# Kernel optimization log

Measured on AMD Instinct MI355X. Metric: run time of the kernel, lower is better.

## Reference

```python
import jax, jax.numpy as jnp
import numpy as np

IN, H, L, T = 44, 128, 4, 50  # input_size, hidden_size, num_layers, target_len
B, S = 2048, 200


def _lstm_cell(xt, h, c, Wih, Whh, b):
    # xt [B,in], h/c [B,H]; Wih [4H,in], Whh [4H,H], b [4H] (b_ih+b_hh fused)
    gates = xt @ Wih.T + h @ Whh.T + b
    i, f, g, o = jnp.split(gates, 4, axis=-1)
    c_new = jax.nn.sigmoid(f) * c + jax.nn.sigmoid(i) * jnp.tanh(g)
    h_new = jax.nn.sigmoid(o) * jnp.tanh(c_new)
    return h_new, c_new


def _run_layer(xs, Wih, Whh, b):
    # xs [S,B,in] -> ys [S,B,H], final (h,c)
    Bn = xs.shape[1]
    h0 = jnp.zeros((Bn, H), xs.dtype)
    c0 = jnp.zeros((Bn, H), xs.dtype)

    def step(carry, xt):
        h, c = carry
        h, c = _lstm_cell(xt, h, c, Wih, Whh, b)
        return (h, c), h

    (hT, cT), ys = jax.lax.scan(step, (h0, c0), xs)
    return ys, hT, cT


def setup_inputs() -> dict:
    key = jax.random.key(0)
    ks = jax.random.split(key, 16)
    s = 1.0 / np.sqrt(H)
    u = lambda k, shape: jax.random.uniform(k, shape, jnp.float32, -s, s)
    return {
        "x": jax.random.normal(ks[0], (B, S, IN), jnp.float32),
        "target": jax.random.normal(ks[1], (B, T, IN), jnp.float32),
        "enc_Wih0": u(ks[2], (4 * H, IN)),
        "enc_WihR": u(ks[3], (L - 1, 4 * H, H)),
        "enc_Whh": u(ks[4], (L, 4 * H, H)),
        "enc_b": u(ks[5], (L, 4 * H)),
        "dec_Wih0": u(ks[6], (4 * H, IN)),
        "dec_WihR": u(ks[7], (L - 1, 4 * H, H)),
        "dec_Whh": u(ks[8], (L, 4 * H, H)),
        "dec_b": u(ks[9], (L, 4 * H)),
        "fc_W": u(ks[10], (IN, H)),
        "fc_b": u(ks[11], (IN,)),
    }


def reference(x, target, enc_Wih0, enc_WihR, enc_Whh, enc_b,
              dec_Wih0, dec_WihR, dec_Whh, dec_b, fc_W, fc_b):
    # ---- encoder: 4-layer LSTM over the source sequence ----
    xs = jnp.transpose(x, (1, 0, 2))  # [S,B,IN]
    ys, h, c = _run_layer(xs, enc_Wih0, enc_Whh[0], enc_b[0])
    hs, cs = [h], [c]
    for l in range(1, L):
        ys, h, c = _run_layer(ys, enc_WihR[l - 1], enc_Whh[l], enc_b[l])
        hs.append(h)
        cs.append(c)
    hs = jnp.stack(hs)  # [L,B,H]
    cs = jnp.stack(cs)

    # ---- decoder: recursive decode for T steps (seq_len=1 per step) ----
    dec_in0 = x[:, -1, :]  # [B,IN]

    def dec_step(carry, _):
        dec_in, hsc, csc = carry
        new_h, new_c = [], []
        inp = dec_in
        for l in range(L):
            Wih = dec_Wih0 if l == 0 else dec_WihR[l - 1]
            hl, cl = _lstm_cell(inp, hsc[l], csc[l], Wih, dec_Whh[l], dec_b[l])
            new_h.append(hl)
            new_c.append(cl)
            inp = hl
        out = inp @ fc_W.T + fc_b  # [B,IN]
        return (out, jnp.stack(new_h), jnp.stack(new_c)), out

    _, outs = jax.lax.scan(dec_step, (dec_in0, hs, cs), None, length=T)
    return jnp.transpose(outs, (1, 0, 2))  # [B,T,IN]
```

## Files before the change

### kernel.cpp

```cpp
#include <hip/hip_runtime.h>
#include <hip/hip_bf16.h>
#include <cstdint>
#include <cstddef>

typedef _Float16 half8  __attribute__((ext_vector_type(8)));
typedef float    floatx4 __attribute__((ext_vector_type(4)));
typedef int      int4v   __attribute__((ext_vector_type(4)));

#define S_LEN 200
#define BATCH 2048
#define HID   128
#define T_LEN 50
#define IN_D  44

#define SENT32 0x7E007E00

#define OFF_ENCW   0ull
#define OFF_DECW   983040ull
#define OFF_RING_E 1978368ull
#define OFF_RING_D 14561280ull
#define OFF_ORING  20852736ull
#define OFF_HENC   21901312ull
#define OFF_CENC   23998464ull
#define OFF_FLAGS  28192768ull

#define SCOPE_AGENT __HIP_MEMORY_SCOPE_AGENT

#define LOG2E  1.44269504f
#define LOG2E2 2.88539008f
__device__ __forceinline__ float sigf(float x){
  float e = __builtin_amdgcn_exp2f(-LOG2E * x);
  return __builtin_amdgcn_rcpf(1.f + e);
}
__device__ __forceinline__ float tanhf_fast(float x){
  float e = __builtin_amdgcn_exp2f(LOG2E2 * x);
  return 1.f - 2.f * __builtin_amdgcn_rcpf(e + 1.f);
}

__device__ __forceinline__ int  ldc(const int* p){ return __hip_atomic_load(p, __ATOMIC_RELAXED, SCOPE_AGENT); }
__device__ __forceinline__ void stc(int* p, int v){ __hip_atomic_store(p, v, __ATOMIC_RELAXED, SCOPE_AGENT); }
__device__ __forceinline__ void drain_vm(){ asm volatile("s_waitcnt vmcnt(0)" ::: "memory"); }
__device__ __forceinline__ int* flagp(int* flags, int idx){ return flags + idx*32; }

__device__ __forceinline__ int4v ld_ring_x4(const int* p){
  int4v r;
  asm volatile("global_load_dwordx4 %0, %1, off sc0 sc1\n\t"
               "s_waitcnt vmcnt(0)"
               : "=v"(r) : "v"(p) : "memory");
  return r;
}
__device__ __forceinline__ void st_ring_x4(int* p, int4v v){
  asm volatile("global_store_dwordx4 %0, %1, off sc0 sc1"
               :: "v"(p), "v"(v) : "memory");
}
__device__ __forceinline__ bool any_sent(int4v v){
  return (v.x==SENT32)||(v.y==SENT32)||(v.z==SENT32)||(v.w==SENT32);
}

#define PIN(v) asm volatile("" : "+v"(v))

__global__ void prep_weights(const float* __restrict__ eW0, const float* __restrict__ eWR,
                             const float* __restrict__ eWH, const float* __restrict__ dW0,
                             const float* __restrict__ dWR, const float* __restrict__ dWH,
                             const float* __restrict__ fcW,
                             _Float16* __restrict__ encw, _Float16* __restrict__ decw,
                             int* __restrict__ rings, int* __restrict__ flags)
{
  int i = blockIdx.x*256 + threadIdx.x;
  if (i < 491520) {
    _Float16 v;
    if (i < 32768)      { int j=i>>6, k=i&63; v = (k<IN_D)? (_Float16)eW0[j*IN_D+k] : (_Float16)0.f; }
    else if (i < 229376){ v = (_Float16)eWR[i-32768]; }
    else                { v = (_Float16)eWH[i-229376]; }
    encw[i] = v;
  }
  if (i < 497664) {
    _Float16 v;
    if (i < 32768)      { int j=i>>6, k=i&63; v = (k<IN_D)? (_Float16)dW0[j*IN_D+k] : (_Float16)0.f; }
    else if (i < 229376){ v = (_Float16)dWR[i-32768]; }
    else if (i < 491520){ v = (_Float16)dWH[i-229376]; }
    else { int r=i-491520; int j=r>>7, k=r&127; v = (j<IN_D)? (_Float16)fcW[j*HID+k] : (_Float16)0.f; }
    decw[i] = v;
  }
  for (int j = i; j < 4980736; j += 4096*256) rings[j] = SENT32;
  if (i < 32768) flags[i] = 0;
}


__global__ __launch_bounds__(512, 2)
void enc_pipe(const float* __restrict__ x, const _Float16* __restrict__ encw,
              const float* __restrict__ enc_b, _Float16* __restrict__ ring,
              _Float16* __restrict__ h_enc, float* __restrict__ c_enc,
              int* __restrict__ flags)
{
  const int tid = threadIdx.x;
  const int w = tid >> 6, lane = tid & 63, quad = lane >> 4, n16 = lane & 15;
  const int l = blockIdx.x >> 6, s = blockIdx.x & 63, r0 = s * 32;
  const int u = w*16 + n16;
  const int KSI = (l == 0) ? 2 : 4;

  __shared__ _Float16 xbuf[32][136];
  __shared__ _Float16 hb[2][32][136];

  for (int i = tid; i < 32*136; i += 512){
    ((_Float16*)xbuf)[i] = (_Float16)0.f;
    ((_Float16*)hb[0])[i] = (_Float16)0.f;
  }

  const _Float16* Wi = (l==0) ? encw : encw + 32768 + (size_t)(l-1)*65536;
  const _Float16* Wh = encw + 229376 + (size_t)l*65536;
  const int KI = KSI * 32;
  floatx4 wfi[4][4], wfh[4][4];
  #pragma unroll
  for (int nt = 0; nt < 4; ++nt){
    const int grow = nt*128 + u;
    #pragma unroll
    for (int ks = 0; ks < 4; ++ks){
      if (ks < KSI){ wfi[nt][ks] = *(const floatx4*)(Wi + (size_t)grow*KI + ks*32 + quad*8); PIN(wfi[nt][ks]); }
      wfh[nt][ks] = *(const floatx4*)(Wh + (size_t)grow*HID + ks*32 + quad*8); PIN(wfh[nt][ks]);
    }
  }
  float breg[4];
  #pragma unroll
  for (int g = 0; g < 4; ++g) breg[g] = enc_b[l*512 + g*128 + u];
  float creg[2][4] = {{0.f,0.f,0.f,0.f},{0.f,0.f,0.f,0.f}};

  int xr_r[3], xr_k[3]; bool xr_v[3]; float xr[3];
  if (l == 0){
    #pragma unroll
    for (int j = 0; j < 3; ++j){
      int idx = tid + j*512; xr_v[j] = idx < 32*IN_D;
      xr_r[j] = xr_v[j] ? idx / IN_D : 0; xr_k[j] = xr_v[j] ? idx % IN_D : 0;
      xr[j] = xr_v[j] ? x[((size_t)(r0+xr_r[j])*S_LEN + 0)*IN_D + xr_k[j]] : 0.f;
    }
  }

  int* cflag_self = flagp(flags, l*64 + s);
  int* cflag_next = flagp(flags, (l+1)*64 + s);
  int seen_cons = 0;

  __syncthreads();

  _Float16 (*hcur)[136] = hb[0];
  _Float16 (*hnxt)[136] = hb[1];

  const int d0 = tid, d1 = tid+512, d2 = tid+1024, d3 = tid+1536;

  for (int t = 0; t < S_LEN; ++t){
    if (l == 0){
      #pragma unroll
      for (int j = 0; j < 3; ++j)
        if (xr_v[j]) xbuf[xr_r[j]][xr_k[j]] = (_Float16)xr[j];
    } else {
      int* srcd = (int*)(ring + (((size_t)(l-1)*8 + (t&7))*BATCH + r0)*HID);
      int v0 = ldc(srcd+d0), v1 = ldc(srcd+d1), v2 = ldc(srcd+d2), v3 = ldc(srcd+d3);
      while (v0==SENT32 || v1==SENT32 || v2==SENT32 || v3==SENT32){
        if (v0==SENT32) v0 = ldc(srcd+d0);
        if (v1==SENT32) v1 = ldc(srcd+d1);
        if (v2==SENT32) v2 = ldc(srcd+d2);
        if (v3==SENT32) v3 = ldc(srcd+d3);
      }
      *(int*)&xbuf[d0>>6][(d0&63)*2] = v0;
      *(int*)&xbuf[d1>>6][(d1&63)*2] = v1;
      *(int*)&xbuf[d2>>6][(d2&63)*2] = v2;
      *(int*)&xbuf[d3>>6][(d3&63)*2] = v3;
      stc(srcd+d0, SENT32); stc(srcd+d1, SENT32);
      stc(srcd+d2, SENT32); stc(srcd+d3, SENT32);
    }
    if (tid == 0 && l < 3 && t >= 8){
      while (seen_cons < t-7){
        seen_cons = ldc(cflag_next);
        if (seen_cons < t-7) __builtin_amdgcn_s_sleep(1);
      }
    }
    __syncthreads();

    if (l == 0 && t < S_LEN-1){
      #pragma unroll
      for (int j = 0; j < 3; ++j)
        if (xr_v[j]) xr[j] = x[((size_t)(r0+xr_r[j])*S_LEN + (t+1))*IN_D + xr_k[j]];
    }

    #pragma unroll
    for (int m = 0; m < 2; ++m){
      half8 ai[4], ah[4];
      #pragma unroll
      for (int ks = 0; ks < 4; ++ks){
        if (ks < KSI) ai[ks] = *(const half8*)&xbuf[m*16+n16][ks*32 + quad*8];
        ah[ks] = *(const half8*)&hcur[m*16+n16][ks*32 + quad*8];
      }
      floatx4 acc[4];
      #pragma unroll
      for (int nt = 0; nt < 4; ++nt){
        acc[nt] = (floatx4){0.f,0.f,0.f,0.f};
        #pragma unroll
        for (int ks = 0; ks < 4; ++ks){
          if (ks < KSI) acc[nt] = __builtin_amdgcn_mfma_f32_16x16x32_f16(ai[ks], __builtin_bit_cast(half8, wfi[nt][ks]), acc[nt], 0,0,0);
          acc[nt] = __builtin_amdgcn_mfma_f32_16x16x32_f16(ah[ks], __builtin_bit_cast(half8, wfh[nt][ks]), acc[nt], 0,0,0);
        }
      }
      #pragma unroll
      for (int rr = 0; rr < 4; ++rr){
        float ip = acc[0][rr] + breg[0];
        float fp = acc[1][rr] + breg[1];
        float gp = acc[2][rr] + breg[2];
        float op = acc[3][rr] + breg[3];
        float cc = sigf(fp)*creg[m][rr] + sigf(ip)*tanhf_fast(gp);
        float hh = sigf(op)*tanhf_fast(cc);
        creg[m][rr] = cc;
        const int row = m*16 + quad*4 + rr;
        hnxt[row][u] = (_Float16)hh;
        if (t == S_LEN-1){
          h_enc[((size_t)l*BATCH + r0 + row)*HID + u] = (_Float16)hh;
          c_enc[((size_t)l*BATCH + r0 + row)*HID + u] = cc;
        }
      }
    }
    __syncthreads();

    if (l > 0){
      drain_vm();
      if (tid == 0) stc(cflag_self, t+1);
    }
    if (l < 3){
      int* dst = (int*)(ring + (((size_t)l*8 + (t&7))*BATCH + r0)*HID);
      stc(dst+d0, *(const int*)&hnxt[d0>>6][(d0&63)*2]);
      stc(dst+d1, *(const int*)&hnxt[d1>>6][(d1&63)*2]);
      stc(dst+d2, *(const int*)&hnxt[d2>>6][(d2&63)*2]);
      stc(dst+d3, *(const int*)&hnxt[d3>>6][(d3&63)*2]);
    }
    _Float16 (*tmp)[136] = hcur; hcur = hnxt; hnxt = tmp;
  }
}


__global__ __launch_bounds__(512, 2)
void dec_pipe(const float* __restrict__ x, const _Float16* __restrict__ decw,
              const float* __restrict__ dec_b, const float* __restrict__ fc_b,
              _Float16* __restrict__ ring, _Float16* __restrict__ oring,
              const _Float16* __restrict__ h_enc, const float* __restrict__ c_enc,
              int* __restrict__ flags, float* __restrict__ out)
{
  const int tid = threadIdx.x;
  const int w = tid >> 6, lane = tid & 63, quad = lane >> 4, n16 = lane & 15;
  const int l = blockIdx.x >> 6, s = blockIdx.x & 63, r0 = s * 32;
  const int u = w*16 + n16;
  const int KSI = (l == 0) ? 2 : 4;
  const int my4 = tid*4;

  __shared__ _Float16 xbuf[32][136];
  __shared__ _Float16 hb[2][32][136];
  __shared__ _Float16 fcout[32][64];

  for (int i = tid; i < 32*136; i += 512) ((_Float16*)xbuf)[i] = (_Float16)0.f;
  for (int i = tid; i < 32*64; i += 512) ((_Float16*)fcout)[i] = (_Float16)0.f;

  const _Float16* Wi = (l==0) ? decw : decw + 32768 + (size_t)(l-1)*65536;
  const _Float16* Wh = decw + 229376 + (size_t)l*65536;
  const _Float16* FCW = decw + 491520;
  const int KI = KSI * 32;
  floatx4 wfi[4][4], wfh[4][4];
  #pragma unroll
  for (int nt = 0; nt < 4; ++nt){
    const int grow = nt*128 + u;
    #pragma unroll
    for (int ks = 0; ks < 4; ++ks){
      if (ks < KSI){ wfi[nt][ks] = *(const floatx4*)(Wi + (size_t)grow*KI + ks*32 + quad*8); PIN(wfi[nt][ks]); }
      wfh[nt][ks] = *(const floatx4*)(Wh + (size_t)grow*HID + ks*32 + quad*8); PIN(wfh[nt][ks]);
    }
  }
  float breg[4];
  #pragma unroll
  for (int g = 0; g < 4; ++g) breg[g] = dec_b[l*512 + g*128 + u];

  {
    int idx = tid*8, rr_ = idx >> 7, kk = idx & 127;
    *(half8*)&hb[0][rr_][kk] = *(const half8*)(h_enc + ((size_t)l*BATCH + r0)*HID + rr_*HID + kk);
  }
  float creg[2][4];
  #pragma unroll
  for (int m = 0; m < 2; ++m)
    #pragma unroll
    for (int rr = 0; rr < 4; ++rr)
      creg[m][rr] = c_enc[((size_t)l*BATCH + r0 + m*16 + quad*4 + rr)*HID + u];

  floatx4 wfc[4]; float fcb_j = 0.f;
  const int j = w*16 + n16;
  if (w < 3){
    #pragma unroll
    for (int ks = 0; ks < 4; ++ks){
      wfc[ks] = *(const floatx4*)(FCW + (size_t)j*HID + ks*32 + quad*8); PIN(wfc[ks]);
    }
    if (j < IN_D) fcb_j = fc_b[j];
  }

  int* cflag_self = flagp(flags, 256 + l*64 + s);
  int* cflag_next = flagp(flags, 256 + (l+1)*64 + s);
  int* cflag_o    = flagp(flags, 512 + s);
  int seen = 0;

  __syncthreads();

  _Float16 (*hcur)[136] = hb[0];
  _Float16 (*hnxt)[136] = hb[1];

  const int4v sv = {SENT32, SENT32, SENT32, SENT32};

  for (int t = 0; t < T_LEN; ++t){
    if (l == 0){
      if (t == 0){
        for (int idx = tid; idx < 32*IN_D; idx += 512){
          int r = idx / IN_D, k = idx % IN_D;
          xbuf[r][k] = (_Float16)x[((size_t)(r0+r)*S_LEN + (S_LEN-1))*IN_D + k];
        }
      } else if (tid < 256){
        int* srcd = (int*)(oring + (((size_t)((t-1)&3))*BATCH + r0)*64);
        int4v v = ld_ring_x4(srcd + my4);
        while (any_sent(v)){
          __builtin_amdgcn_s_sleep(1);
          v = ld_ring_x4(srcd + my4);
        }
        *(int4v*)&xbuf[my4>>5][(my4&31)*2] = v;
        st_ring_x4(srcd + my4, sv);
      }
    } else {
      int* srcd = (int*)(ring + (((size_t)(l-1)*4 + (t&3))*BATCH + r0)*HID);
      int4v v = ld_ring_x4(srcd + my4);
      while (any_sent(v)){
        __builtin_amdgcn_s_sleep(1);
        v = ld_ring_x4(srcd + my4);
      }
      *(int4v*)&xbuf[my4>>6][(my4&63)*2] = v;
      st_ring_x4(srcd + my4, sv);
    }
    if (tid == 0 && t >= 4){
      if (l < 3){
        while (seen < t-3){ seen = ldc(cflag_next); if (seen < t-3) __builtin_amdgcn_s_sleep(1); }
      } else {
        while (seen < t-2){ seen = ldc(cflag_o); if (seen < t-2) __builtin_amdgcn_s_sleep(1); }
      }
    }
    __syncthreads();

    #pragma unroll
    for (int m = 0; m < 2; ++m){
      half8 ai[4], ah[4];
      #pragma unroll
      for (int ks = 0; ks < 4; ++ks){
        if (ks < KSI) ai[ks] = *(const half8*)&xbuf[m*16+n16][ks*32 + quad*8];
        ah[ks] = *(const half8*)&hcur[m*16+n16][ks*32 + quad*8];
      }
      floatx4 acc[4];
      #pragma unroll
      for (int nt = 0; nt < 4; ++nt){
        acc[nt] = (floatx4){0.f,0.f,0.f,0.f};
        #pragma unroll
        for (int ks = 0; ks < 4; ++ks){
          if (ks < KSI) acc[nt] = __builtin_amdgcn_mfma_f32_16x16x32_f16(ai[ks], __builtin_bit_cast(half8, wfi[nt][ks]), acc[nt], 0,0,0);
          acc[nt] = __builtin_amdgcn_mfma_f32_16x16x32_f16(ah[ks], __builtin_bit_cast(half8, wfh[nt][ks]), acc[nt], 0,0,0);
        }
      }
      #pragma unroll
      for (int rr = 0; rr < 4; ++rr){
        float ip = acc[0][rr] + breg[0];
        float fp = acc[1][rr] + breg[1];
        float gp = acc[2][rr] + breg[2];
        float op = acc[3][rr] + breg[3];
        float cc = sigf(fp)*creg[m][rr] + sigf(ip)*tanhf_fast(gp);
        float hh = sigf(op)*tanhf_fast(cc);
        creg[m][rr] = cc;
        hnxt[m*16 + quad*4 + rr][u] = (_Float16)hh;
      }
    }
    __syncthreads();

    drain_vm();
    if (tid == 0){
      if (l > 0) stc(cflag_self, t+1);
      else if (t > 0) stc(cflag_o, t+1);
    }

    if (l < 3){
      int* dst = (int*)(ring + (((size_t)l*4 + (t&3))*BATCH + r0)*HID);
      st_ring_x4(dst + my4, *(const int4v*)&hnxt[my4>>6][(my4&63)*2]);
    } else {
      if (w < 3){
        #pragma unroll
        for (int m = 0; m < 2; ++m){
          half8 a3[4];
          #pragma unroll
          for (int ks = 0; ks < 4; ++ks) a3[ks] = *(const half8*)&hnxt[m*16+n16][ks*32 + quad*8];
          floatx4 facc = (floatx4){0.f,0.f,0.f,0.f};
          #pragma unroll
          for (int ks = 0; ks < 4; ++ks) facc = __builtin_amdgcn_mfma_f32_16x16x32_f16(a3[ks], __builtin_bit_cast(half8, wfc[ks]), facc, 0,0,0);
          #pragma unroll
          for (int rr = 0; rr < 4; ++rr){
            const int row = m*16 + quad*4 + rr;
            float v = facc[rr] + fcb_j;
            fcout[row][j] = (_Float16)v;
            if (j < IN_D)
              out[((size_t)(r0 + row)*T_LEN + t)*IN_D + j] = v;
          }
        }
      }
      __syncthreads();
      if (tid < 256){
        int* odst = (int*)(oring + (((size_t)(t&3))*BATCH + r0)*64);
        st_ring_x4(odst + my4, *(const int4v*)&fcout[my4>>5][(my4&31)*2]);
      }
    }
    _Float16 (*tmp)[136] = hcur; hcur = hnxt; hnxt = tmp;
  }
  drain_vm();
}

extern "C" void kernel_launch(void* const* d_in, const int* in_sizes, int n_in,
                              void* d_out, int out_size, void* d_ws, size_t ws_size,
                              hipStream_t stream)
{
  const float* x        = (const float*)d_in[0];
  const float* enc_Wih0 = (const float*)d_in[2];
  const float* enc_WihR = (const float*)d_in[3];
  const float* enc_Whh  = (const float*)d_in[4];
  const float* enc_b    = (const float*)d_in[5];
  const float* dec_Wih0 = (const float*)d_in[6];
  const float* dec_WihR = (const float*)d_in[7];
  const float* dec_Whh  = (const float*)d_in[8];
  const float* dec_b    = (const float*)d_in[9];
  const float* fc_W     = (const float*)d_in[10];
  const float* fc_b     = (const float*)d_in[11];

  char* ws = (char*)d_ws;
  _Float16* encw   = (_Float16*)(ws + OFF_ENCW);
  _Float16* decw   = (_Float16*)(ws + OFF_DECW);
  _Float16* ring_e = (_Float16*)(ws + OFF_RING_E);
  _Float16* ring_d = (_Float16*)(ws + OFF_RING_D);
  _Float16* oring  = (_Float16*)(ws + OFF_ORING);
  _Float16* h_enc  = (_Float16*)(ws + OFF_HENC);
  float*    c_enc  = (float*)(ws + OFF_CENC);
  int*      flags  = (int*)(ws + OFF_FLAGS);
  int*      rings  = (int*)(ws + OFF_RING_E);
  float*    outp   = (float*)d_out;

  prep_weights<<<4096, 256, 0, stream>>>(enc_Wih0, enc_WihR, enc_Whh,
                                         dec_Wih0, dec_WihR, dec_Whh, fc_W,
                                         encw, decw, rings, flags);
  enc_pipe<<<256, 512, 0, stream>>>(x, encw, enc_b, ring_e, h_enc, c_enc, flags);
  dec_pipe<<<256, 512, 0, stream>>>(x, decw, dec_b, fc_b, ring_d, oring,
                                    h_enc, c_enc, flags, outp);
}
```

Baseline: 1.432 ms.

## Process two encoder timesteps per ring handoff with vectorized ring loads and stores

The encoder pipeline now consumes and produces two timesteps per iteration, so inter-layer ring polling, sentinel resets and consumer-flag handshakes happen half as often. Ring traffic uses 16-byte vector loads and stores per thread instead of four scalar 4-byte accesses, and the input buffer is double-buffered for the pair. The cost is extra pipeline latency between layers, since a layer waits for two steps from its producer, plus a sleep inside the poll loop that could add wake-up delay.

```diff
diff --git a/kernel.cpp b/kernel.cpp
--- a/kernel.cpp
+++ b/kernel.cpp
@@ -98,13 +98,17 @@
   const int l = blockIdx.x >> 6, s = blockIdx.x & 63, r0 = s * 32;
   const int u = w*16 + n16;
   const int KSI = (l == 0) ? 2 : 4;
-
-  __shared__ _Float16 xbuf[32][136];
-  __shared__ _Float16 hb[2][32][136];
+  const int my4 = tid*4;
+
+  __shared__ _Float16 xb[2][32][136];
+  __shared__ _Float16 hA[32][136];
+  __shared__ _Float16 hB[32][136];
 
   for (int i = tid; i < 32*136; i += 512){
-    ((_Float16*)xbuf)[i] = (_Float16)0.f;
-    ((_Float16*)hb[0])[i] = (_Float16)0.f;
+    ((_Float16*)xb[0])[i] = (_Float16)0.f;
+    ((_Float16*)xb[1])[i] = (_Float16)0.f;
+    ((_Float16*)hA)[i] = (_Float16)0.f;
+    ((_Float16*)hB)[i] = (_Float16)0.f;
   }
 
   const _Float16* Wi = (l==0) ? encw : encw + 32768 + (size_t)(l-1)*65536;
@@ -125,13 +129,15 @@
   for (int g = 0; g < 4; ++g) breg[g] = enc_b[l*512 + g*128 + u];
   float creg[2][4] = {{0.f,0.f,0.f,0.f},{0.f,0.f,0.f,0.f}};
 
-  int xr_r[3], xr_k[3]; bool xr_v[3]; float xr[3];
+  int xr_r[3], xr_k[3]; bool xr_v[3]; float xr[2][3];
   if (l == 0){
     #pragma unroll
     for (int j = 0; j < 3; ++j){
       int idx = tid + j*512; xr_v[j] = idx < 32*IN_D;
       xr_r[j] = xr_v[j] ? idx / IN_D : 0; xr_k[j] = xr_v[j] ? idx % IN_D : 0;
-      xr[j] = xr_v[j] ? x[((size_t)(r0+xr_r[j])*S_LEN + 0)*IN_D + xr_k[j]] : 0.f;
+      #pragma unroll
+      for (int p = 0; p < 2; ++p)
+        xr[p][j] = xr_v[j] ? x[((size_t)(r0+xr_r[j])*S_LEN + p)*IN_D + xr_k[j]] : 0.f;
     }
   }
 
@@ -139,55 +145,15 @@
   int* cflag_next = flagp(flags, (l+1)*64 + s);
   int seen_cons = 0;
 
-  __syncthreads();
-
-  _Float16 (*hcur)[136] = hb[0];
-  _Float16 (*hnxt)[136] = hb[1];
-
-  const int d0 = tid, d1 = tid+512, d2 = tid+1024, d3 = tid+1536;
-
-  for (int t = 0; t < S_LEN; ++t){
-    if (l == 0){
-      #pragma unroll
-      for (int j = 0; j < 3; ++j)
-        if (xr_v[j]) xbuf[xr_r[j]][xr_k[j]] = (_Float16)xr[j];
-    } else {
-      int* srcd = (int*)(ring + (((size_t)(l-1)*8 + (t&7))*BATCH + r0)*HID);
-      int v0 = ldc(srcd+d0), v1 = ldc(srcd+d1), v2 = ldc(srcd+d2), v3 = ldc(srcd+d3);
-      while (v0==SENT32 || v1==SENT32 || v2==SENT32 || v3==SENT32){
-        if (v0==SENT32) v0 = ldc(srcd+d0);
-        if (v1==SENT32) v1 = ldc(srcd+d1);
-        if (v2==SENT32) v2 = ldc(srcd+d2);
-        if (v3==SENT32) v3 = ldc(srcd+d3);
-      }
-      *(int*)&xbuf[d0>>6][(d0&63)*2] = v0;
-      *(int*)&xbuf[d1>>6][(d1&63)*2] = v1;
-      *(int*)&xbuf[d2>>6][(d2&63)*2] = v2;
-      *(int*)&xbuf[d3>>6][(d3&63)*2] = v3;
-      stc(srcd+d0, SENT32); stc(srcd+d1, SENT32);
-      stc(srcd+d2, SENT32); stc(srcd+d3, SENT32);
-    }
-    if (tid == 0 && l < 3 && t >= 8){
-      while (seen_cons < t-7){
-        seen_cons = ldc(cflag_next);
-        if (seen_cons < t-7) __builtin_amdgcn_s_sleep(1);
-      }
-    }
-    __syncthreads();
-
-    if (l == 0 && t < S_LEN-1){
-      #pragma unroll
-      for (int j = 0; j < 3; ++j)
-        if (xr_v[j]) xr[j] = x[((size_t)(r0+xr_r[j])*S_LEN + (t+1))*IN_D + xr_k[j]];
-    }
-
+  auto cell = [&](const _Float16 (*xin)[136], const _Float16 (*hin)[136],
+                  _Float16 (*hout)[136], bool writeHC){
     #pragma unroll
     for (int m = 0; m < 2; ++m){
       half8 ai[4], ah[4];
       #pragma unroll
       for (int ks = 0; ks < 4; ++ks){
-        if (ks < KSI) ai[ks] = *(const half8*)&xbuf[m*16+n16][ks*32 + quad*8];
-        ah[ks] = *(const half8*)&hcur[m*16+n16][ks*32 + quad*8];
+        if (ks < KSI) ai[ks] = *(const half8*)&xin[m*16+n16][ks*32 + quad*8];
+        ah[ks] = *(const half8*)&hin[m*16+n16][ks*32 + quad*8];
       }
       floatx4 acc[4];
       #pragma unroll
@@ -209,28 +175,73 @@
         float hh = sigf(op)*tanhf_fast(cc);
         creg[m][rr] = cc;
         const int row = m*16 + quad*4 + rr;
-        hnxt[row][u] = (_Float16)hh;
-        if (t == S_LEN-1){
+        hout[row][u] = (_Float16)hh;
+        if (writeHC){
           h_enc[((size_t)l*BATCH + r0 + row)*HID + u] = (_Float16)hh;
           c_enc[((size_t)l*BATCH + r0 + row)*HID + u] = cc;
         }
       }
     }
+  };
+
+  __syncthreads();
+
+  const int4v sv = {SENT32, SENT32, SENT32, SENT32};
+
+  for (int q = 0; q < S_LEN/2; ++q){
+    if (l == 0){
+      #pragma unroll
+      for (int p = 0; p < 2; ++p)
+        #pragma unroll
+        for (int j = 0; j < 3; ++j)
+          if (xr_v[j]) xb[p][xr_r[j]][xr_k[j]] = (_Float16)xr[p][j];
+    } else {
+      const int sbase = (l-1)*8 + ((q&3)<<1);
+      int* s0 = (int*)(ring + ((size_t)(sbase+0)*BATCH + r0)*HID) + my4;
+      int* s1 = (int*)(ring + ((size_t)(sbase+1)*BATCH + r0)*HID) + my4;
+      int4v v0 = ld_ring_x4(s0);
+      while (any_sent(v0)){ __builtin_amdgcn_s_sleep(1); v0 = ld_ring_x4(s0); }
+      int4v v1 = ld_ring_x4(s1);
+      while (any_sent(v1)){ __builtin_amdgcn_s_sleep(1); v1 = ld_ring_x4(s1); }
+      *(int4v*)&xb[0][my4>>6][(my4&63)*2] = v0;
+      *(int4v*)&xb[1][my4>>6][(my4&63)*2] = v1;
+      st_ring_x4(s0, sv);
+      st_ring_x4(s1, sv);
+    }
+    if (tid == 0 && l < 3 && q >= 4){
+      while (seen_cons < q-3){
+        seen_cons = ldc(cflag_next);
+        if (seen_cons < q-3) __builtin_amdgcn_s_sleep(1);
+      }
+    }
+    __syncthreads();
+
+    if (l == 0 && q < S_LEN/2 - 1){
+      #pragma unroll
+      for (int p = 0; p < 2; ++p)
+        #pragma unroll
+        for (int j = 0; j < 3; ++j)
+          if (xr_v[j]) xr[p][j] = x[((size_t)(r0+xr_r[j])*S_LEN + (2*q+2+p))*IN_D + xr_k[j]];
+    }
+
+    cell(xb[0], hA, hB, false);
+    __syncthreads();
+    cell(xb[1], hB, hA, (q == S_LEN/2 - 1));
     __syncthreads();
 
     if (l > 0){
       drain_vm();
-      if (tid == 0) stc(cflag_self, t+1);
+      if (tid == 0) stc(cflag_self, q+1);
     }
     if (l < 3){
-      int* dst = (int*)(ring + (((size_t)l*8 + (t&7))*BATCH + r0)*HID);
-      stc(dst+d0, *(const int*)&hnxt[d0>>6][(d0&63)*2]);
-      stc(dst+d1, *(const int*)&hnxt[d1>>6][(d1&63)*2]);
-      stc(dst+d2, *(const int*)&hnxt[d2>>6][(d2&63)*2]);
-      stc(dst+d3, *(const int*)&hnxt[d3>>6][(d3&63)*2]);
-    }
-    _Float16 (*tmp)[136] = hcur; hcur = hnxt; hnxt = tmp;
-  }
+      const int dbase = l*8 + ((q&3)<<1);
+      int* d0p = (int*)(ring + ((size_t)(dbase+0)*BATCH + r0)*HID) + my4;
+      int* d1p = (int*)(ring + ((size_t)(dbase+1)*BATCH + r0)*HID) + my4;
+      st_ring_x4(d0p, *(const int4v*)&hB[my4>>6][(my4&63)*2]);
+      st_ring_x4(d1p, *(const int4v*)&hA[my4>>6][(my4&63)*2]);
+    }
+  }
+  drain_vm();
 }
 
 
```

After: 1.301 ms. 1.1x faster.
